# Optimization experiments

Measured on AMD Instinct MI355X. Metric: run time of the kernel, lower is better.

Reference implementation:

```python
import jax, jax.numpy as jnp
import numpy as np

V, D, H, B, LA, LC = 50000, 300, 256, 32, 256, 256


def setup_inputs():
    key = jax.random.key(0)
    ks = jax.random.split(key, 20)
    u = lambda k, sh, sc: jax.random.uniform(k, sh, jnp.float32, -sc, sc)
    s = 1.0 / float(np.sqrt(H))
    return {
        "anchor_input": jax.random.randint(ks[0], (B, LA), 0, V),
        "anchor_length": jax.random.randint(ks[1], (B,), 1, LA + 1),
        "candidate_input": jax.random.randint(ks[2], (B, LC), 0, V),
        "candidate_length": jax.random.randint(ks[3], (B,), 1, LC + 1),
        "batch_size": B,
        "emb": jax.random.normal(ks[4], (V, D), jnp.float32) * 0.1,
        "W_ih_a": u(ks[5], (3 * H, D), s),
        "W_hh_a": u(ks[6], (3 * H, H), s),
        "b_ih_a": u(ks[7], (3 * H,), s),
        "b_hh_a": u(ks[8], (3 * H,), s),
        "W_ih_c": u(ks[9], (3 * H, D + H), s),
        "W_hh_c": u(ks[10], (3 * H, H), s),
        "b_ih_c": u(ks[11], (3 * H,), s),
        "b_hh_c": u(ks[12], (3 * H,), s),
        "Wq": u(ks[13], (H, H), s),
        "Wk": u(ks[14], (H, H), s),
        "v_att": u(ks[15], (H,), s),
    }


def _gru_step(x, h, W_ih, W_hh, b_ih, b_hh):
    # torch GRUCell convention (gate order r, z, n)
    gi = x @ W_ih.T + b_ih
    gh = h @ W_hh.T + b_hh
    ir, iz, inn = jnp.split(gi, 3, axis=-1)
    hr, hz, hn = jnp.split(gh, 3, axis=-1)
    r = jax.nn.sigmoid(ir + hr)
    z = jax.nn.sigmoid(iz + hz)
    n = jnp.tanh(inn + r * hn)
    return (1.0 - z) * n + z * h


def _forward(anchor_input, anchor_length, candidate_input, candidate_length,
             emb, W_ih_a, W_hh_a, b_ih_a, b_hh_a,
             W_ih_c, W_hh_c, b_ih_c, b_hh_c, Wq, Wk, v_att):
    Bb = anchor_input.shape[0]
    # ---- anchor encoder: GRU with packed-sequence semantics (zero pad outputs, freeze hidden) ----
    ax = emb[anchor_input].transpose(1, 0, 2)  # [LA, B, D]
    ts_a = jnp.arange(ax.shape[0])

    def a_step(h, inp):
        xt, t = inp
        hn = _gru_step(xt, h, W_ih_a, W_hh_a, b_ih_a, b_hh_a)
        valid = (t < anchor_length)[:, None]
        h = jnp.where(valid, hn, h)
        return h, jnp.where(valid, hn, 0.0)

    h0 = jnp.zeros((Bb, H), ax.dtype)
    anchor_hidden, a_outs = jax.lax.scan(a_step, h0, (ax, ts_a))  # a_outs: [LA, B, H]
    anchor_outputs = a_outs.transpose(1, 0, 2)  # [B, LA, H]
    anchor_emb = a_outs.sum(0) / anchor_length.astype(ax.dtype)[:, None]  # meanVector

    # ---- candidate decoder: per-step additive attention + GRU + length-mask blend ----
    keys = anchor_outputs @ Wk  # [B, LA, H], precomputed once
    cx = emb[candidate_input].transpose(1, 0, 2)  # [LC, B, D]
    ts_c = jnp.arange(cx.shape[0])

    def c_step(h, inp):
        xt, t = inp
        q = h @ Wq  # [B, H] query from previous hidden
        scores = jnp.einsum('blh,h->bl', jnp.tanh(keys + q[:, None, :]), v_att)
        attn = jax.nn.softmax(scores, axis=-1)
        context = jnp.einsum('bl,blh->bh', attn, anchor_outputs)
        hn = _gru_step(jnp.concatenate([xt, context], axis=-1), h,
                       W_ih_c, W_hh_c, b_ih_c, b_hh_c)
        mask = (candidate_length < t).astype(h.dtype)[:, None]  # strict '<' is faithful to source
        h = hn * (1.0 - mask) + mask * h
        return h, h * (1.0 - mask)

    _, c_outs = jax.lax.scan(c_step, anchor_hidden, (cx, ts_c))  # [LC, B, H]
    valid_c = (ts_c[:, None] < candidate_length[None, :]).astype(cx.dtype)[:, :, None]
    candidate_emb = (c_outs * valid_c).sum(0) / candidate_length.astype(cx.dtype)[:, None]
    return anchor_emb, candidate_emb


def reference(anchor_input, anchor_length, candidate_input, candidate_length, batch_size,
              emb, W_ih_a, W_hh_a, b_ih_a, b_hh_a,
              W_ih_c, W_hh_c, b_ih_c, b_hh_c, Wq, Wk, v_att):
    return _forward(anchor_input, anchor_length, candidate_input, candidate_length,
                    emb, W_ih_a, W_hh_a, b_ih_a, b_hh_a,
                    W_ih_c, W_hh_c, b_ih_c, b_hh_c, Wq, Wk, v_att)
```

## Files before the change

kernel.cpp:

```cpp
#include <hip/hip_runtime.h>
#include <hip/hip_fp16.h>
#include <math.h>

#define BB 32
#define LAV 256
#define LCV 256
#define DV 300
#define HV 256
#define G3 768

typedef _Float16 f16x2 __attribute__((ext_vector_type(2)));
union F4H8 { float4 f4; f16x2 h2[4]; };
union U2H4 { uint2 u2; f16x2 h2[2]; };

static __device__ __forceinline__ float rcp_(float x) { return __builtin_amdgcn_rcpf(x); }
static __device__ __forceinline__ float sigm(float x) { return rcp_(1.f + __expf(-x)); }
static __device__ __forceinline__ float tanh_(float x) { return 1.f - 2.f * rcp_(1.f + __expf(2.f * x)); }

__global__ void prep_pack(const float* __restrict__ W_ih_a, const float* __restrict__ W_ih_c,
                          const float* __restrict__ W_hh_a, const float* __restrict__ W_hh_c,
                          const float* __restrict__ Wq,
                          float* __restrict__ WT_a, float* __restrict__ WT_cx,
                          __half* __restrict__ WhaRH, __half* __restrict__ WhaSH,
                          __half* __restrict__ WqH, __half* __restrict__ WrzH,
                          __half* __restrict__ WnH)
{
    int i = blockIdx.x * 256 + threadIdx.x;
    switch (blockIdx.y) {
    case 0: if (i < 230400) { int k = i / 768, n = i % 768; WT_a[i] = W_ih_a[n * 300 + k]; } break;
    case 1: if (i < 230400) { int k = i / 768, n = i % 768; WT_cx[i] = W_ih_c[n * 556 + k]; } break;
    case 2: if (i < 98304) { int e = i & 1, r = i >> 1, ii = r & 63, j = r >> 6;
            WhaRH[i] = __float2half(W_hh_a[j * 256 + 2 * ii + e]); } break;
    case 3: if (i < 98304) { int e = i & 1, s = (i >> 1) & 1, r = i >> 2, j = r % 768, i2 = r / 768;
            int k = 2 * (64 + 2 * i2 + s) + e;
            WhaSH[i] = __float2half(W_hh_a[j * 256 + k]); } break;
    case 4: if (i < 65536) { int e = i & 1, r2 = i >> 1, m = r2 & 255, k2 = r2 >> 8;
            WqH[i] = __float2half(Wq[(2 * k2 + e) * 256 + m]); } break;
    case 5: if (i < 262144) { int e = i & 1, r2 = i >> 1, j = r2 & 511, kk = r2 >> 9;
            int kh = kk >> 7, k2i = kk & 127, k = kh * 256 + 2 * k2i + e;
            float v = (k < 256) ? W_hh_c[j * 256 + k] : W_ih_c[j * 556 + 300 + (k - 256)];
            WrzH[i] = __float2half(v); } break;
    case 6: if (i < 131072) { int e = i & 1, r2 = i >> 1, j = r2 & 255, gg = r2 >> 8;
            int slot = gg >> 6, k2i = gg & 63, grp = slot >> 1, kh = slot & 1;
            int kl = kh * 128 + 2 * k2i + e;
            float v = grp ? W_ih_c[(512 + j) * 556 + 300 + kl] : W_hh_c[(512 + j) * 256 + kl];
            WnH[i] = __float2half(v); } break;
    }
}

template <int MODE>
__global__ __launch_bounds__(256) void gemm_tile(
    const float* __restrict__ X, const int* __restrict__ gidx, int ldx,
    const float* __restrict__ Wt, int K, int Nn,
    const float* __restrict__ bias, float* __restrict__ Cout)
{
    __shared__ __align__(16) float As[32][68];
    __shared__ __align__(16) float Bs[32][68];
    __shared__ int toks[64];
    int tid = threadIdx.x;
    int m0 = blockIdx.x * 64, n0 = blockIdx.y * 64;
    if (tid < 64) {
        int m = m0 + tid;
        if (gidx) { int t = m >> 5, b = m & 31; toks[tid] = gidx[b * LAV + t]; }
        else toks[tid] = m;
    }
    __syncthreads();
    float acc[4][4] = {};
    int tx = tid & 15, ty = tid >> 4;
    for (int k0 = 0; k0 < K; k0 += 32) {
        {
            int r = tid >> 2, cc = (tid & 3) * 8;
            const float* src = X + (size_t)toks[r] * ldx + k0 + cc;
            float4 v0 = {0.f,0.f,0.f,0.f}, v1 = {0.f,0.f,0.f,0.f};
            if (k0 + cc + 3 < K) v0 = *(const float4*)src;
            if (k0 + cc + 7 < K) v1 = *(const float4*)(src + 4);
            As[cc+0][r]=v0.x; As[cc+1][r]=v0.y; As[cc+2][r]=v0.z; As[cc+3][r]=v0.w;
            As[cc+4][r]=v1.x; As[cc+5][r]=v1.y; As[cc+6][r]=v1.z; As[cc+7][r]=v1.w;
        }
        {
            int kr = tid >> 4, c4 = (tid & 15) * 4;
            #pragma unroll
            for (int p = 0; p < 2; ++p) {
                float4 v = {0.f,0.f,0.f,0.f};
                int kg = k0 + kr + p * 16;
                if (kg < K) v = *(const float4*)(Wt + (size_t)kg * Nn + n0 + c4);
                *(float4*)&Bs[kr + p * 16][c4] = v;
            }
        }
        __syncthreads();
        #pragma unroll 8
        for (int kk = 0; kk < 32; ++kk) {
            float4 a4 = *(const float4*)&As[kk][ty * 4];
            float4 b4 = *(const float4*)&Bs[kk][tx * 4];
            acc[0][0]=fmaf(a4.x,b4.x,acc[0][0]); acc[0][1]=fmaf(a4.x,b4.y,acc[0][1]);
            acc[0][2]=fmaf(a4.x,b4.z,acc[0][2]); acc[0][3]=fmaf(a4.x,b4.w,acc[0][3]);
            acc[1][0]=fmaf(a4.y,b4.x,acc[1][0]); acc[1][1]=fmaf(a4.y,b4.y,acc[1][1]);
            acc[1][2]=fmaf(a4.y,b4.z,acc[1][2]); acc[1][3]=fmaf(a4.y,b4.w,acc[1][3]);
            acc[2][0]=fmaf(a4.z,b4.x,acc[2][0]); acc[2][1]=fmaf(a4.z,b4.y,acc[2][1]);
            acc[2][2]=fmaf(a4.z,b4.z,acc[2][2]); acc[2][3]=fmaf(a4.z,b4.w,acc[2][3]);
            acc[3][0]=fmaf(a4.w,b4.x,acc[3][0]); acc[3][1]=fmaf(a4.w,b4.y,acc[3][1]);
            acc[3][2]=fmaf(a4.w,b4.z,acc[3][2]); acc[3][3]=fmaf(a4.w,b4.w,acc[3][3]);
        }
        __syncthreads();
    }
    if (MODE == 0) {
        float4 bz = *(const float4*)&bias[n0 + tx * 4];
        #pragma unroll
        for (int i = 0; i < 4; ++i) {
            int m = m0 + ty * 4 + i;
            float4 o = { acc[i][0] + bz.x, acc[i][1] + bz.y, acc[i][2] + bz.z, acc[i][3] + bz.w };
            *(float4*)&Cout[(size_t)m * Nn + n0 + tx * 4] = o;
        }
    } else {
        int b_ = m0 >> 8;
        int l0 = (m0 & 255) + ty * 4;
        f16x2* TH = (f16x2*)Cout;
        #pragma unroll
        for (int j = 0; j < 4; ++j) {
            int h = n0 + tx * 4 + j;
            size_t base = ((size_t)(b_ * 256 + h)) * 128 + (l0 >> 1);
            f16x2 v01 = { (_Float16)tanh_(acc[0][j]), (_Float16)tanh_(acc[1][j]) };
            f16x2 v23 = { (_Float16)tanh_(acc[2][j]), (_Float16)tanh_(acc[3][j]) };
            TH[base] = v01;
            TH[base + 1] = v23;
        }
    }
}

__global__ __launch_bounds__(768) void anchor_rnn(
    const float* __restrict__ GI, const int* __restrict__ lens,
    const float* __restrict__ bhh, const __half* __restrict__ WhaRH,
    const __half* __restrict__ WhaSH,
    float* __restrict__ AO, __half* __restrict__ AOH,
    float* __restrict__ hid, float* __restrict__ outp)
{
    __shared__ float gh[768];
    __shared__ __align__(16) float hs[256];
    __shared__ __align__(16) f16x2 hx2[128];
    __shared__ float bhhS[768];
    int bid = blockIdx.x, tid = threadIdx.x;
    int len = lens[bid];

    f16x2 wreg[64];
    {
        const float4* s = (const float4*)WhaRH + (size_t)tid * 16;
        #pragma unroll
        for (int u = 0; u < 16; ++u) {
            F4H8 c; c.f4 = s[u];
            wreg[4*u+0] = c.h2[0]; wreg[4*u+1] = c.h2[1];
            wreg[4*u+2] = c.h2[2]; wreg[4*u+3] = c.h2[3];
        }
    }
    if (tid < 256) hs[tid] = 0.f;
    if (tid < 128) { f16x2 z = {(_Float16)0.f, (_Float16)0.f}; hx2[tid] = z; }
    bhhS[tid] = bhh[tid];
    float sum = 0.f;
    __syncthreads();

    for (int t = 0; t < LAV; ++t) {
        {
            float a0=0.f,a1=0.f,a2=0.f,a3=0.f;
            const float4* xb = (const float4*)hx2;
            #pragma unroll
            for (int u = 0; u < 16; ++u) {
                F4H8 xv; xv.f4 = xb[u];
                a0 = __builtin_amdgcn_fdot2(wreg[4*u+0], xv.h2[0], a0, false);
                a1 = __builtin_amdgcn_fdot2(wreg[4*u+1], xv.h2[1], a1, false);
                a2 = __builtin_amdgcn_fdot2(wreg[4*u+2], xv.h2[2], a2, false);
                a3 = __builtin_amdgcn_fdot2(wreg[4*u+3], xv.h2[3], a3, false);
            }
            const uint2* wsp = (const uint2*)WhaSH + tid;
            float b0=0.f,b1=0.f;
            #pragma unroll
            for (int i2 = 0; i2 < 32; ++i2) {
                U2H4 w; w.u2 = wsp[(size_t)i2 * 768];
                U2H4 xx; xx.u2 = *(const uint2*)&hx2[64 + 2 * i2];
                b0 = __builtin_amdgcn_fdot2(w.h2[0], xx.h2[0], b0, false);
                b1 = __builtin_amdgcn_fdot2(w.h2[1], xx.h2[1], b1, false);
            }
            gh[tid] = ((a0 + a1) + (a2 + a3)) + (b0 + b1) + bhhS[tid];
        }
        __syncthreads();
        if (tid < 256) {
            const float* gi = GI + ((size_t)t * BB + bid) * G3;
            float r = sigm(gi[tid] + gh[tid]);
            float z = sigm(gi[256 + tid] + gh[256 + tid]);
            float n = tanh_(fmaf(r, gh[512 + tid], gi[512 + tid]));
            float hk = hs[tid];
            float hn = (1.f - z) * n + z * hk;
            bool valid = (t < len);
            float hnew = valid ? hn : hk;
            hs[tid] = hnew;
            float ov = valid ? hn : 0.f;
            AO[((size_t)bid * LAV + t) * HV + tid] = ov;
            AOH[((size_t)bid * LAV + t) * HV + tid] = __float2half(ov);
            sum += ov;
            float other = __shfl_xor(hnew, 1, 64);
            if (!(tid & 1)) {
                f16x2 v = { (_Float16)hnew, (_Float16)other };
                hx2[tid >> 1] = v;
            }
        }
        __syncthreads();
    }
    if (tid < 256) {
        outp[bid * HV + tid] = sum / (float)len;
        hid[bid * HV + tid] = hs[tid];
    }
}

__global__ __launch_bounds__(1024) void cand_rnn(
    const float* __restrict__ GI, const int* __restrict__ lens,
    const float* __restrict__ bhh, const __half* __restrict__ WrzH,
    const __half* __restrict__ WnH, const __half* __restrict__ WqH,
    const float* __restrict__ v_att, const __half* __restrict__ AOH,
    const __half* __restrict__ TH, const float* __restrict__ hid,
    float* __restrict__ outp)
{
    __shared__ __align__(16) f16x2 x2[256];
    __shared__ __align__(16) float hs[256];
    __shared__ float tqs[256];
    __shared__ float vls[256];
    __shared__ float attn[256];
    __shared__ __align__(16) float redBig[2048];
    __shared__ __align__(16) float redRZh[1024];
    __shared__ __align__(16) float redNh[1024];
    __shared__ float bhhS[768];
    __shared__ float wred[8];

    int tid = threadIdx.x;
    int b = blockIdx.x;
    int len = lens[b];

    const f16x2* Wq2  = (const f16x2*)WqH;
    const f16x2* Wrz2 = (const f16x2*)WrzH;
    const f16x2* Wn2  = (const f16x2*)WnH;
    const f16x2* T2   = (const f16x2*)TH + (size_t)b * 256 * 128;
    const f16x2* AO2  = (const f16x2*)AOH + (size_t)b * 256 * 128;

    if (tid < 256) { hs[tid] = hid[b * HV + tid]; vls[tid] = v_att[tid]; }
    if (tid < 768) bhhS[tid] = bhh[tid];
    __syncthreads();
    if (tid < 128) {
        f16x2 v = { (_Float16)hs[2 * tid], (_Float16)hs[2 * tid + 1] };
        x2[tid] = v;
    }
    __syncthreads();

    float csum = 0.f;

    for (int t = 0; t < LCV; ++t) {
        {
            int m = tid & 255, kc = tid >> 8;
            float a0 = 0.f, a1 = 0.f;
            #pragma unroll 8
            for (int i = 0; i < 32; i += 2) {
                int k2 = kc * 32 + i;
                a0 = __builtin_amdgcn_fdot2(Wq2[k2 * 256 + m], x2[k2], a0, false);
                a1 = __builtin_amdgcn_fdot2(Wq2[(k2 + 1) * 256 + m], x2[k2 + 1], a1, false);
            }
            redBig[kc * 256 + m] = a0 + a1;
        }
        {
            int j = tid & 511, kh2 = tid >> 9;
            float a0 = 0.f, a1 = 0.f;
            #pragma unroll 8
            for (int i = 0; i < 64; i += 2) {
                int kk = kh2 * 64 + i;
                a0 = __builtin_amdgcn_fdot2(Wrz2[(size_t)kk * 512 + j], x2[kk], a0, false);
                a1 = __builtin_amdgcn_fdot2(Wrz2[(size_t)(kk + 1) * 512 + j], x2[kk + 1], a1, false);
            }
            redRZh[tid] = a0 + a1;
        }
        {
            int j = tid & 255, q4 = tid >> 8;
            float a0 = 0.f, a1 = 0.f;
            #pragma unroll 8
            for (int i = 0; i < 32; i += 2) {
                int gg = q4 * 32 + i;
                a0 = __builtin_amdgcn_fdot2(Wn2[(size_t)gg * 256 + j], x2[gg], a0, false);
                a1 = __builtin_amdgcn_fdot2(Wn2[(size_t)(gg + 1) * 256 + j], x2[gg + 1], a1, false);
            }
            redNh[tid] = a0 + a1;
        }
        __syncthreads();
        if (tid < 256) {
            float q = redBig[tid] + redBig[256 + tid] + redBig[512 + tid] + redBig[768 + tid];
            tqs[tid] = tanh_(q);
        }
        __syncthreads();
        {
            int l2 = tid & 127, hg = tid >> 7;
            float s0 = 0.f, s1 = 0.f;
            #pragma unroll 8
            for (int i = 0; i < 32; ++i) {
                int h = hg * 32 + i;
                f16x2 Tv = T2[(size_t)h * 128 + l2];
                float tq = tqs[h], vv = vls[h];
                float T0 = (float)Tv.x, T1 = (float)Tv.y;
                float d0 = fmaxf(fmaf(T0, tq, 1.f), 1e-6f);
                float d1 = fmaxf(fmaf(T1, tq, 1.f), 1e-6f);
                s0 = fmaf(vv * (T0 + tq), rcp_(d0), s0);
                s1 = fmaf(vv * (T1 + tq), rcp_(d1), s1);
            }
            redBig[hg * 256 + 2 * l2] = s0;
            redBig[hg * 256 + 2 * l2 + 1] = s1;
        }
        __syncthreads();
        if (tid < 256) {
            float sv = 0.f;
            #pragma unroll
            for (int hg = 0; hg < 8; ++hg) sv += redBig[hg * 256 + tid];
            float e = __expf(sv);
            attn[tid] = e;
            float s = e;
            #pragma unroll
            for (int o = 1; o < 64; o <<= 1) s += __shfl_xor(s, o, 64);
            if ((tid & 63) == 0) wred[4 + (tid >> 6)] = s;
        }
        __syncthreads();
        {
            int ho2 = tid & 127, lc = tid >> 7;
            float c0 = 0.f, c1 = 0.f;
            #pragma unroll 8
            for (int i = 0; i < 32; ++i) {
                int l = lc * 32 + i;
                f16x2 ao = AO2[(size_t)l * 128 + ho2];
                float w = attn[l];
                c0 = fmaf(w, (float)ao.x, c0);
                c1 = fmaf(w, (float)ao.y, c1);
            }
            redBig[lc * 256 + 2 * ho2] = c0;
            redBig[lc * 256 + 2 * ho2 + 1] = c1;
        }
        __syncthreads();
        if (tid < 128) {
            float c0 = 0.f, c1 = 0.f;
            #pragma unroll
            for (int lc = 0; lc < 8; ++lc) {
                c0 += redBig[lc * 256 + 2 * tid];
                c1 += redBig[lc * 256 + 2 * tid + 1];
            }
            float rs = rcp_(wred[4] + wred[5] + wred[6] + wred[7]);
            f16x2 v = { (_Float16)(c0 * rs), (_Float16)(c1 * rs) };
            x2[128 + tid] = v;
        }
        __syncthreads();
        {
            int j = tid & 511, kh2 = tid >> 9;
            float a0 = 0.f, a1 = 0.f;
            #pragma unroll 8
            for (int i = 0; i < 64; i += 2) {
                int kk = 128 + kh2 * 64 + i;
                a0 = __builtin_amdgcn_fdot2(Wrz2[(size_t)kk * 512 + j], x2[kk], a0, false);
                a1 = __builtin_amdgcn_fdot2(Wrz2[(size_t)(kk + 1) * 512 + j], x2[kk + 1], a1, false);
            }
            redBig[tid] = a0 + a1;
        }
        {
            int j = tid & 255, q4 = tid >> 8;
            float a0 = 0.f, a1 = 0.f;
            #pragma unroll 8
            for (int i = 0; i < 32; i += 2) {
                int gg = 128 + q4 * 32 + i;
                a0 = __builtin_amdgcn_fdot2(Wn2[(size_t)gg * 256 + j], x2[gg], a0, false);
                a1 = __builtin_amdgcn_fdot2(Wn2[(size_t)(gg + 1) * 256 + j], x2[gg + 1], a1, false);
            }
            redBig[1024 + tid] = a0 + a1;
        }
        __syncthreads();
        if (tid < 256) {
            const float* gi = GI + ((size_t)t * BB + b) * G3;
            float rr = (redRZh[tid] + redRZh[512 + tid]) + (redBig[tid] + redBig[512 + tid]);
            float zz = (redRZh[256 + tid] + redRZh[768 + tid]) + (redBig[256 + tid] + redBig[768 + tid]);
            float nh = (redNh[tid] + redNh[256 + tid]) + (redNh[512 + tid] + redNh[768 + tid]);
            float nc = (redBig[1024 + tid] + redBig[1280 + tid]) + (redBig[1536 + tid] + redBig[1792 + tid]);
            float r = sigm(gi[tid] + rr + bhhS[tid]);
            float z = sigm(gi[256 + tid] + zz + bhhS[256 + tid]);
            float n = tanh_(gi[512 + tid] + nc + r * (nh + bhhS[512 + tid]));
            float hk = hs[tid];
            float hn = (1.f - z) * n + z * hk;
            float hnew = (len < t) ? hk : hn;
            hs[tid] = hnew;
            if (t < len) csum += hnew;
            float other = __shfl_xor(hnew, 1, 64);
            if ((tid & 1) == 0) {
                f16x2 v = { (_Float16)hnew, (_Float16)other };
                x2[tid >> 1] = v;
            }
        }
        __syncthreads();
    }
    if (tid < 256) outp[8192 + b * HV + tid] = csum / (float)len;
}

extern "C" void kernel_launch(void* const* d_in, const int* in_sizes, int n_in,
                              void* d_out, int out_size, void* d_ws, size_t ws_size,
                              hipStream_t stream) {
    const int* anchor_input     = (const int*)d_in[0];
    const int* anchor_length    = (const int*)d_in[1];
    const int* candidate_input  = (const int*)d_in[2];
    const int* candidate_length = (const int*)d_in[3];
    const float* emb    = (const float*)d_in[5];
    const float* W_ih_a = (const float*)d_in[6];
    const float* W_hh_a = (const float*)d_in[7];
    const float* b_ih_a = (const float*)d_in[8];
    const float* b_hh_a = (const float*)d_in[9];
    const float* W_ih_c = (const float*)d_in[10];
    const float* W_hh_c = (const float*)d_in[11];
    const float* b_ih_c = (const float*)d_in[12];
    const float* b_hh_c = (const float*)d_in[13];
    const float* Wq     = (const float*)d_in[14];
    const float* Wk     = (const float*)d_in[15];
    const float* v_att  = (const float*)d_in[16];
    float* out = (float*)d_out;

    float* ws = (float*)d_ws;
    size_t off = 0;
    float* GI_a  = ws + off; off += (size_t)LAV * BB * G3;
    float* GI_c  = ws + off; off += (size_t)LCV * BB * G3;
    float* AO    = ws + off; off += (size_t)BB * LAV * HV;
    float* hid   = ws + off; off += (size_t)BB * HV;
    float* WT_a  = ws + off; off += 300 * 768;
    float* WT_cx = ws + off; off += 300 * 768;
    __half* TH    = (__half*)(ws + off); off += (size_t)BB * HV * LAV / 2;
    __half* AOH   = (__half*)(ws + off); off += (size_t)BB * LAV * HV / 2;
    __half* WhaRH = (__half*)(ws + off); off += 98304 / 2;
    __half* WhaSH = (__half*)(ws + off); off += 98304 / 2;
    __half* WqH   = (__half*)(ws + off); off += 65536 / 2;
    __half* WrzH  = (__half*)(ws + off); off += 262144 / 2;
    __half* WnH   = (__half*)(ws + off); off += 131072 / 2;

    prep_pack<<<dim3(1024, 7), 256, 0, stream>>>(W_ih_a, W_ih_c, W_hh_a, W_hh_c, Wq,
                                                 WT_a, WT_cx, WhaRH, WhaSH, WqH, WrzH, WnH);
    gemm_tile<0><<<dim3(128, 12), 256, 0, stream>>>(emb, anchor_input, DV, WT_a, DV, G3, b_ih_a, GI_a);
    gemm_tile<0><<<dim3(128, 12), 256, 0, stream>>>(emb, candidate_input, DV, WT_cx, DV, G3, b_ih_c, GI_c);
    anchor_rnn<<<32, 768, 0, stream>>>(GI_a, anchor_length, b_hh_a, WhaRH, WhaSH, AO, AOH, hid, out);
    gemm_tile<1><<<dim3(128, 4), 256, 0, stream>>>(AO, nullptr, HV, Wk, HV, HV, nullptr, (float*)TH);
    cand_rnn<<<32, 1024, 0, stream>>>(GI_c, candidate_length, b_hh_c, WrzH, WnH, WqH,
                                      v_att, AOH, TH, hid, out);
}
```

Before: 3.837 ms.

## Precompute anchor outputs times context input weights to fold attention context into gates

A new GEMM multiplies the anchor outputs by the context slice of W_ih_c ahead of time, producing per-position gate projections P stored in fp16. Each candidate step can then compute the context contribution to the gates as attention weights times P. This replaces the per-step weighted sum over anchor outputs plus the context-weight matvec, removing two reduction phases and their barriers. Softmax now subtracts the max for stability. In exchange, each step reads a 768-wide P row per position instead of a 256-wide one, and the extra GEMM writes into the reused GI_a buffer.

Result: no change. 3.907 ms (+1.8%).

```diff
diff --git a/kernel.cpp b/kernel.cpp
--- a/kernel.cpp
+++ b/kernel.cpp
@@ -23,7 +23,7 @@
                           float* __restrict__ WT_a, float* __restrict__ WT_cx,
                           __half* __restrict__ WhaRH, __half* __restrict__ WhaSH,
                           __half* __restrict__ WqH, __half* __restrict__ WrzH,
-                          __half* __restrict__ WnH)
+                          __half* __restrict__ WnH, float* __restrict__ WcxCT)
 {
     int i = blockIdx.x * 256 + threadIdx.x;
     switch (blockIdx.y) {
@@ -45,6 +45,8 @@
             int kl = kh * 128 + 2 * k2i + e;
             float v = grp ? W_ih_c[(512 + j) * 556 + 300 + kl] : W_hh_c[(512 + j) * 256 + kl];
             WnH[i] = __float2half(v); } break;
+    case 7: if (i < 196608) { int k = i / 768, j = i % 768;
+            WcxCT[i] = W_ih_c[j * 556 + 300 + k]; } break;
     }
 }
 
@@ -111,7 +113,7 @@
             float4 o = { acc[i][0] + bz.x, acc[i][1] + bz.y, acc[i][2] + bz.z, acc[i][3] + bz.w };
             *(float4*)&Cout[(size_t)m * Nn + n0 + tx * 4] = o;
         }
-    } else {
+    } else if (MODE == 1) {
         int b_ = m0 >> 8;
         int l0 = (m0 & 255) + ty * 4;
         f16x2* TH = (f16x2*)Cout;
@@ -123,6 +125,17 @@
             f16x2 v23 = { (_Float16)tanh_(acc[2][j]), (_Float16)tanh_(acc[3][j]) };
             TH[base] = v01;
             TH[base + 1] = v23;
+        }
+    } else {
+        int l0 = m0 + ty * 4;
+        f16x2* P2 = (f16x2*)Cout;
+        #pragma unroll
+        for (int j = 0; j < 4; ++j) {
+            int col = n0 + tx * 4 + j;
+            f16x2 v01 = { (_Float16)acc[0][j], (_Float16)acc[1][j] };
+            f16x2 v23 = { (_Float16)acc[2][j], (_Float16)acc[3][j] };
+            P2[(size_t)(l0 >> 1) * 768 + col] = v01;
+            P2[(size_t)((l0 >> 1) + 1) * 768 + col] = v23;
         }
     }
 }
@@ -213,18 +226,19 @@
     const float* __restrict__ GI, const int* __restrict__ lens,
     const float* __restrict__ bhh, const __half* __restrict__ WrzH,
     const __half* __restrict__ WnH, const __half* __restrict__ WqH,
-    const float* __restrict__ v_att, const __half* __restrict__ AOH,
+    const float* __restrict__ v_att, const __half* __restrict__ P2H,
     const __half* __restrict__ TH, const float* __restrict__ hid,
     float* __restrict__ outp)
 {
-    __shared__ __align__(16) f16x2 x2[256];
+    __shared__ __align__(16) f16x2 x2[128];
     __shared__ __align__(16) float hs[256];
     __shared__ float tqs[256];
     __shared__ float vls[256];
-    __shared__ float attn[256];
+    __shared__ __align__(4) __half attnH[256];
     __shared__ __align__(16) float redBig[2048];
     __shared__ __align__(16) float redRZh[1024];
     __shared__ __align__(16) float redNh[1024];
+    __shared__ __align__(16) float gateC[768];
     __shared__ float bhhS[768];
     __shared__ float wred[8];
 
@@ -236,7 +250,7 @@
     const f16x2* Wrz2 = (const f16x2*)WrzH;
     const f16x2* Wn2  = (const f16x2*)WnH;
     const f16x2* T2   = (const f16x2*)TH + (size_t)b * 256 * 128;
-    const f16x2* AO2  = (const f16x2*)AOH + (size_t)b * 256 * 128;
+    const f16x2* P2b  = (const f16x2*)P2H + (size_t)b * 128 * 768;
 
     if (tid < 256) { hs[tid] = hid[b * HV + tid]; vls[tid] = v_att[tid]; }
     if (tid < 768) bhhS[tid] = bhh[tid];
@@ -307,74 +321,44 @@
             redBig[hg * 256 + 2 * l2 + 1] = s1;
         }
         __syncthreads();
+        float sv = 0.f;
         if (tid < 256) {
-            float sv = 0.f;
             #pragma unroll
             for (int hg = 0; hg < 8; ++hg) sv += redBig[hg * 256 + tid];
-            float e = __expf(sv);
-            attn[tid] = e;
+            float m = sv;
+            #pragma unroll
+            for (int o = 1; o < 64; o <<= 1) m = fmaxf(m, __shfl_xor(m, o, 64));
+            if ((tid & 63) == 0) wred[tid >> 6] = m;
+        }
+        __syncthreads();
+        if (tid < 256) {
+            float mx = fmaxf(fmaxf(wred[0], wred[1]), fmaxf(wred[2], wred[3]));
+            float e = __expf(sv - mx);
+            attnH[tid] = __float2half(e);
             float s = e;
             #pragma unroll
             for (int o = 1; o < 64; o <<= 1) s += __shfl_xor(s, o, 64);
             if ((tid & 63) == 0) wred[4 + (tid >> 6)] = s;
         }
         __syncthreads();
-        {
-            int ho2 = tid & 127, lc = tid >> 7;
-            float c0 = 0.f, c1 = 0.f;
-            #pragma unroll 8
-            for (int i = 0; i < 32; ++i) {
-                int l = lc * 32 + i;
-                f16x2 ao = AO2[(size_t)l * 128 + ho2];
-                float w = attn[l];
-                c0 = fmaf(w, (float)ao.x, c0);
-                c1 = fmaf(w, (float)ao.y, c1);
-            }
-            redBig[lc * 256 + 2 * ho2] = c0;
-            redBig[lc * 256 + 2 * ho2 + 1] = c1;
-        }
-        __syncthreads();
-        if (tid < 128) {
-            float c0 = 0.f, c1 = 0.f;
-            #pragma unroll
-            for (int lc = 0; lc < 8; ++lc) {
-                c0 += redBig[lc * 256 + 2 * tid];
-                c1 += redBig[lc * 256 + 2 * tid + 1];
-            }
-            float rs = rcp_(wred[4] + wred[5] + wred[6] + wred[7]);
-            f16x2 v = { (_Float16)(c0 * rs), (_Float16)(c1 * rs) };
-            x2[128 + tid] = v;
-        }
-        __syncthreads();
-        {
-            int j = tid & 511, kh2 = tid >> 9;
+        if (tid < 768) {
+            const f16x2* at2 = (const f16x2*)attnH;
             float a0 = 0.f, a1 = 0.f;
             #pragma unroll 8
-            for (int i = 0; i < 64; i += 2) {
-                int kk = 128 + kh2 * 64 + i;
-                a0 = __builtin_amdgcn_fdot2(Wrz2[(size_t)kk * 512 + j], x2[kk], a0, false);
-                a1 = __builtin_amdgcn_fdot2(Wrz2[(size_t)(kk + 1) * 512 + j], x2[kk + 1], a1, false);
-            }
-            redBig[tid] = a0 + a1;
-        }
-        {
-            int j = tid & 255, q4 = tid >> 8;
-            float a0 = 0.f, a1 = 0.f;
-            #pragma unroll 8
-            for (int i = 0; i < 32; i += 2) {
-                int gg = 128 + q4 * 32 + i;
-                a0 = __builtin_amdgcn_fdot2(Wn2[(size_t)gg * 256 + j], x2[gg], a0, false);
-                a1 = __builtin_amdgcn_fdot2(Wn2[(size_t)(gg + 1) * 256 + j], x2[gg + 1], a1, false);
-            }
-            redBig[1024 + tid] = a0 + a1;
+            for (int l2 = 0; l2 < 128; l2 += 2) {
+                a0 = __builtin_amdgcn_fdot2(P2b[(size_t)l2 * 768 + tid], at2[l2], a0, false);
+                a1 = __builtin_amdgcn_fdot2(P2b[(size_t)(l2 + 1) * 768 + tid], at2[l2 + 1], a1, false);
+            }
+            gateC[tid] = a0 + a1;
         }
         __syncthreads();
         if (tid < 256) {
             const float* gi = GI + ((size_t)t * BB + b) * G3;
-            float rr = (redRZh[tid] + redRZh[512 + tid]) + (redBig[tid] + redBig[512 + tid]);
-            float zz = (redRZh[256 + tid] + redRZh[768 + tid]) + (redBig[256 + tid] + redBig[768 + tid]);
+            float rs = rcp_(wred[4] + wred[5] + wred[6] + wred[7]);
+            float rr = (redRZh[tid] + redRZh[512 + tid]) + gateC[tid] * rs;
+            float zz = (redRZh[256 + tid] + redRZh[768 + tid]) + gateC[256 + tid] * rs;
             float nh = (redNh[tid] + redNh[256 + tid]) + (redNh[512 + tid] + redNh[768 + tid]);
-            float nc = (redBig[1024 + tid] + redBig[1280 + tid]) + (redBig[1536 + tid] + redBig[1792 + tid]);
+            float nc = gateC[512 + tid] * rs;
             float r = sigm(gi[tid] + rr + bhhS[tid]);
             float z = sigm(gi[256 + tid] + zz + bhhS[256 + tid]);
             float n = tanh_(gi[512 + tid] + nc + r * (nh + bhhS[512 + tid]));
@@ -430,13 +414,16 @@
     __half* WqH   = (__half*)(ws + off); off += 65536 / 2;
     __half* WrzH  = (__half*)(ws + off); off += 262144 / 2;
     __half* WnH   = (__half*)(ws + off); off += 131072 / 2;
-
-    prep_pack<<<dim3(1024, 7), 256, 0, stream>>>(W_ih_a, W_ih_c, W_hh_a, W_hh_c, Wq,
-                                                 WT_a, WT_cx, WhaRH, WhaSH, WqH, WrzH, WnH);
+    float* WcxCT  = ws + off; off += 256 * 768;
+    __half* P2H = (__half*)GI_a;
+
+    prep_pack<<<dim3(1024, 8), 256, 0, stream>>>(W_ih_a, W_ih_c, W_hh_a, W_hh_c, Wq,
+                                                 WT_a, WT_cx, WhaRH, WhaSH, WqH, WrzH, WnH, WcxCT);
     gemm_tile<0><<<dim3(128, 12), 256, 0, stream>>>(emb, anchor_input, DV, WT_a, DV, G3, b_ih_a, GI_a);
     gemm_tile<0><<<dim3(128, 12), 256, 0, stream>>>(emb, candidate_input, DV, WT_cx, DV, G3, b_ih_c, GI_c);
     anchor_rnn<<<32, 768, 0, stream>>>(GI_a, anchor_length, b_hh_a, WhaRH, WhaSH, AO, AOH, hid, out);
     gemm_tile<1><<<dim3(128, 4), 256, 0, stream>>>(AO, nullptr, HV, Wk, HV, HV, nullptr, (float*)TH);
+    gemm_tile<2><<<dim3(128, 12), 256, 0, stream>>>(AO, nullptr, HV, WcxCT, HV, G3, nullptr, (float*)P2H);
     cand_rnn<<<32, 1024, 0, stream>>>(GI_c, candidate_length, b_hh_c, WrzH, WnH, WqH,
-                                      v_att, AOH, TH, hid, out);
+                                      v_att, P2H, TH, hid, out);
 }
```
